# Kernel optimization log

Measured on AMD Instinct MI355X. Metric: run time of the kernel, lower is better.

The kernel has to match this reference:

```python
import jax, jax.numpy as jnp
import numpy as np

B, N, C_IN, D, K = 4, 512, 256, 256, 20


def setup_inputs() -> dict:
    key = jax.random.key(0)
    ks = jax.random.split(key, 6)
    s_in = 1.0 / np.sqrt(C_IN)
    return {
        "x": jax.random.normal(ks[0], (B, N, C_IN), dtype=jnp.float32),
        "edge_index": jnp.zeros((2, 4), dtype=jnp.int64),
        "batch": jnp.zeros((B * N,), dtype=jnp.int64),
        "W_l": jax.random.uniform(ks[1], (D, C_IN), jnp.float32, -s_in, s_in),
        "b_l": jax.random.uniform(ks[2], (D,), jnp.float32, -s_in, s_in),
        "W_r": jax.random.uniform(ks[3], (D, C_IN), jnp.float32, -s_in, s_in),
        "b_r": jax.random.uniform(ks[4], (D,), jnp.float32, -s_in, s_in),
        "att": jax.random.normal(ks[5], (1, D), dtype=jnp.float32) * 0.1,
    }


def reference(x, edge_index, batch, W_l, b_l, W_r, b_r, att):
    b, n, _ = x.shape
    k = K
    # linear projections -> [b, n, d]
    x_l = jnp.einsum("bnc,dc->bnd", x, W_l) + b_l
    x_r = jnp.einsum("bnc,dc->bnd", x, W_r) + b_r
    # pairwise additive attention: [b, n, n, d]
    pair = x_l[:, :, None, :] + x_r[:, None, :, :]
    pair = jnp.where(pair >= 0, pair, 0.2 * pair)  # leaky_relu(0.2)
    alpha = jnp.einsum("bijd,d->bij", pair, att[0])  # [b, n, n]
    alpha = jnp.nan_to_num(alpha, nan=0.0, posinf=0.0, neginf=0.0)
    # knn reduction: topk over last dim
    attention, indices = jax.lax.top_k(alpha, k)  # [b, n, k]
    attention = jax.nn.softmax(attention, axis=-1).reshape(-1)  # [b*n*k]
    # edge index construction with per-batch node offsets
    offset = (jnp.arange(b, dtype=indices.dtype) * n)[:, None]  # [b, 1]
    index_i = jnp.repeat(jnp.arange(n, dtype=indices.dtype), k)[None, :] + offset
    index_j = indices.reshape(b, n * k) + offset
    new_edge_index = jnp.stack([index_i.reshape(-1), index_j.reshape(-1)], axis=0)
    # dropout is identity in eval mode; learn_sys=False -> return directly
    return new_edge_index, attention
```

## Files before the change

kernel.cpp:

```cpp
#include <hip/hip_runtime.h>
#include <math.h>


#define GLD_LDS(gp, lp)                                                        \
    __builtin_amdgcn_global_load_lds(                                          \
        (const __attribute__((address_space(1))) float*)(gp),                  \
        (__attribute__((address_space(3))) float*)(lp), 16, 0, 0)

__global__ __launch_bounds__(256) void k_transpose(const float* __restrict__ x,
        const float* __restrict__ Wl, const float* __restrict__ Wr,
        float* __restrict__ WtL, float* __restrict__ WtR, float* __restrict__ xT) {
    const int g = blockIdx.x, c = threadIdx.x;
    if (g < 256)      WtL[c * 256 + g] = Wl[g * 256 + c];
    else if (g < 512) WtR[c * 256 + (g - 256)] = Wr[(g - 256) * 256 + c];
    else {
        const int r = g - 512;
        xT[(size_t)c * 2048 + r] = x[(size_t)r * 256 + c];
    }
}

__global__ __launch_bounds__(256, 1) void k_proj(const float* __restrict__ xT,
        const float* __restrict__ WtL, const float* __restrict__ WtR,
        const float* __restrict__ bl, const float* __restrict__ br,
        float* __restrict__ XL, float* __restrict__ XRt) {
    __shared__ __align__(16) float xst[256 * 64];
    __shared__ __align__(16) float wst[256 * 64];
    const int tid = threadIdx.x;
    const int lane = tid & 63;
    const int wv = tid >> 6;
    const int g = blockIdx.x;
    const int side = g & 1;
    const int dq = (g >> 1) & 3;
    const int rb = g >> 3;
    const int R = rb * 64;
    const int d0 = dq * 64;
    const int b = R >> 9;
    const float* __restrict__ W = side ? WtR : WtL;

#pragma unroll
    for (int n = 0; n < 16; ++n) {
        const int f4 = (n * 4 + wv) * 64 + lane;
        const int c = f4 >> 4, k4 = f4 & 15;
        GLD_LDS(xT + (size_t)c * 2048 + R + k4 * 4, &xst[(n * 4 + wv) * 256]);
        GLD_LDS(W + (size_t)c * 256 + d0 + k4 * 4, &wst[(n * 4 + wv) * 256]);
    }
    __syncthreads();

    const int rt = tid & 15;
    const int dt = tid >> 4;
    float acc[4][4];
#pragma unroll
    for (int r = 0; r < 4; ++r)
#pragma unroll
        for (int k = 0; k < 4; ++k) acc[r][k] = 0.f;

    const float* xp = &xst[rt * 4];
    const float* wp = &wst[dt * 4];
#pragma unroll 8
    for (int c = 0; c < 256; ++c) {
        const float4 xv = *(const float4*)(xp + c * 64);
        const float4 wq = *(const float4*)(wp + c * 64);
#define PROJ_R(r, XS)                              \
        acc[r][0] = fmaf(XS, wq.x, acc[r][0]);     \
        acc[r][1] = fmaf(XS, wq.y, acc[r][1]);     \
        acc[r][2] = fmaf(XS, wq.z, acc[r][2]);     \
        acc[r][3] = fmaf(XS, wq.w, acc[r][3]);
        PROJ_R(0, xv.x)
        PROJ_R(1, xv.y)
        PROJ_R(2, xv.z)
        PROJ_R(3, xv.w)
#undef PROJ_R
    }

    const float4 bias = *(const float4*)&(side ? br : bl)[d0 + dt * 4];
    if (side == 0) {
#pragma unroll
        for (int r = 0; r < 4; ++r) {
            *(float4*)&XL[(size_t)(R + rt * 4 + r) * 256 + d0 + dt * 4] =
                make_float4(acc[r][0] + bias.x, acc[r][1] + bias.y,
                            acc[r][2] + bias.z, acc[r][3] + bias.w);
        }
    } else {
        const int jr = (R & 511) + rt * 4;
#pragma unroll
        for (int k = 0; k < 4; ++k) {
            const int d = d0 + dt * 4 + k;
            const float bk = k == 0 ? bias.x : k == 1 ? bias.y : k == 2 ? bias.z : bias.w;
            *(float4*)&XRt[((size_t)(b * 256 + d)) * 512 + jr] =
                make_float4(acc[0][k] + bk, acc[1][k] + bk,
                            acc[2][k] + bk, acc[3][k] + bk);
        }
    }
}

__global__ __launch_bounds__(512, 2) void k_pair_topk(const float* __restrict__ XL,
        const float* __restrict__ XRt, const float* __restrict__ att,
        float* __restrict__ out) {
    __shared__ __align__(16) float xls[8 * 256];
    __shared__ __align__(16) float atts[256];
    __shared__ __align__(16) float mrg[3 * 4096];
    __shared__ __align__(16) float mrgb[3 * 512];
    __shared__ float Ais[8];
    const int tid = threadIdx.x;
    const int jc = tid & 127;
    const int h = tid >> 7;
    const int g = blockIdx.x;
    const int R = g * 8, b = R >> 9;

    ((float4*)xls)[tid] = ((const float4*)(XL + (size_t)R * 256))[tid];
    if (tid < 64) ((float4*)atts)[tid] = ((const float4*)att)[tid];
    __syncthreads();

    if (tid < 64) {
        const int ii = tid >> 3, seg = tid & 7;
        const float* xp2 = &xls[ii * 256 + seg * 32];
        const float* ap2 = &atts[seg * 32];
        float p = 0.f;
#pragma unroll
        for (int q = 0; q < 8; ++q) {
            const float4 xv = *(const float4*)(xp2 + q * 4);
            const float4 av = *(const float4*)(ap2 + q * 4);
            p += av.x * xv.x + av.y * xv.y + av.z * xv.z + av.w * xv.w;
        }
        p += __shfl_xor(p, 1); p += __shfl_xor(p, 2); p += __shfl_xor(p, 4);
        if (seg == 0) Ais[ii] = p;
    }

    const int dbase = h * 64;
    const float* __restrict__ xrp = XRt + (size_t)b * 131072 + (size_t)dbase * 512 + jc * 4;

    float acc[8][4];
#pragma unroll
    for (int i = 0; i < 8; ++i)
#pragma unroll
        for (int c = 0; c < 4; ++c) acc[i][c] = 0.f;
    float bacc[4] = {0.f, 0.f, 0.f, 0.f};

    float4 bufA[8], bufB[8];
#pragma unroll
    for (int dd = 0; dd < 8; ++dd) bufA[dd] = *(const float4*)(xrp + (size_t)dd * 512);

#pragma unroll
    for (int ch = 0; ch < 8; ++ch) {
        const float4* cur = (ch & 1) ? bufB : bufA;
        float4* nxt = (ch & 1) ? bufA : bufB;
        if (ch < 7) {
            const float* p = xrp + (size_t)(ch + 1) * 8 * 512;
#pragma unroll
            for (int dd = 0; dd < 8; ++dd) nxt[dd] = *(const float4*)(p + (size_t)dd * 512);
        }
        const int d0 = dbase + ch * 8;
        const float4 at0 = *(const float4*)&atts[d0];
        const float4 at1 = *(const float4*)&atts[d0 + 4];
#define BSTEP(ATC, XR4)                                    \
        bacc[0] = fmaf(ATC, XR4.x, bacc[0]);               \
        bacc[1] = fmaf(ATC, XR4.y, bacc[1]);               \
        bacc[2] = fmaf(ATC, XR4.z, bacc[2]);               \
        bacc[3] = fmaf(ATC, XR4.w, bacc[3]);
        BSTEP(at0.x, cur[0]) BSTEP(at0.y, cur[1]) BSTEP(at0.z, cur[2]) BSTEP(at0.w, cur[3])
        BSTEP(at1.x, cur[4]) BSTEP(at1.y, cur[5]) BSTEP(at1.z, cur[6]) BSTEP(at1.w, cur[7])
#undef BSTEP
#pragma unroll
        for (int i = 0; i < 8; ++i) {
            const float4 xa = *(const float4*)&xls[i * 256 + d0];
            const float4 xb = *(const float4*)&xls[i * 256 + d0 + 4];
#define PSTEP(XLC, ATC, XR4)                                       \
            acc[i][0] = fmaf(ATC, fabsf(XLC + XR4.x), acc[i][0]);   \
            acc[i][1] = fmaf(ATC, fabsf(XLC + XR4.y), acc[i][1]);   \
            acc[i][2] = fmaf(ATC, fabsf(XLC + XR4.z), acc[i][2]);   \
            acc[i][3] = fmaf(ATC, fabsf(XLC + XR4.w), acc[i][3]);
            PSTEP(xa.x, at0.x, cur[0])
            PSTEP(xa.y, at0.y, cur[1])
            PSTEP(xa.z, at0.z, cur[2])
            PSTEP(xa.w, at0.w, cur[3])
            PSTEP(xb.x, at1.x, cur[4])
            PSTEP(xb.y, at1.y, cur[5])
            PSTEP(xb.z, at1.z, cur[6])
            PSTEP(xb.w, at1.w, cur[7])
#undef PSTEP
        }
    }

    if (h) {
        float* m = &mrg[(h - 1) * 4096];
#pragma unroll
        for (int i = 0; i < 8; ++i)
            *(float4*)&m[i * 512 + jc * 4] =
                make_float4(acc[i][0], acc[i][1], acc[i][2], acc[i][3]);
        *(float4*)&mrgb[(h - 1) * 512 + jc * 4] =
            make_float4(bacc[0], bacc[1], bacc[2], bacc[3]);
    }
    __syncthreads();
    if (h == 0) {
        const float4 bm0 = *(const float4*)&mrgb[jc * 4];
        const float4 bm1 = *(const float4*)&mrgb[512 + jc * 4];
        const float4 bm2 = *(const float4*)&mrgb[1024 + jc * 4];
        const float Bf0 = bacc[0] + bm0.x + bm1.x + bm2.x;
        const float Bf1 = bacc[1] + bm0.y + bm1.y + bm2.y;
        const float Bf2 = bacc[2] + bm0.z + bm1.z + bm2.z;
        const float Bf3 = bacc[3] + bm0.w + bm1.w + bm2.w;
#pragma unroll
        for (int i = 0; i < 8; ++i) {
            const float Ai = Ais[i];
            const float4 m0 = *(const float4*)&mrg[i * 512 + jc * 4];
            const float4 m1 = *(const float4*)&mrg[4096 + i * 512 + jc * 4];
            const float4 m2 = *(const float4*)&mrg[8192 + i * 512 + jc * 4];
            float a0 = fmaf(0.4f, acc[i][0] + m0.x + m1.x + m2.x, 0.6f * (Ai + Bf0));
            float a1 = fmaf(0.4f, acc[i][1] + m0.y + m1.y + m2.y, 0.6f * (Ai + Bf1));
            float a2 = fmaf(0.4f, acc[i][2] + m0.z + m1.z + m2.z, 0.6f * (Ai + Bf2));
            float a3 = fmaf(0.4f, acc[i][3] + m0.w + m1.w + m2.w, 0.6f * (Ai + Bf3));
            if (!isfinite(a0)) a0 = 0.f;
            if (!isfinite(a1)) a1 = 0.f;
            if (!isfinite(a2)) a2 = 0.f;
            if (!isfinite(a3)) a3 = 0.f;
            *(float4*)&mrg[i * 512 + jc * 4] = make_float4(a0, a1, a2, a3);
        }
    }
    __syncthreads();

    const int lane = tid & 63;
    const int i = tid >> 6;
    const float* ar = &mrg[i * 512];
    const float4 u0 = *(const float4*)&ar[lane * 8];
    const float4 u1 = *(const float4*)&ar[lane * 8 + 4];
    float v[8] = {u0.x, u0.y, u0.z, u0.w, u1.x, u1.y, u1.z, u1.w};

    float myval = 0.f, mmax = 0.f;
    int myidx = 0;
    for (int sel = 0; sel < 20; ++sel) {
        float bv = v[0]; int bt = 0;
#pragma unroll
        for (int t = 1; t < 8; ++t) { if (v[t] > bv) { bv = v[t]; bt = t; } }
        int bj = lane * 8 + bt;
#pragma unroll
        for (int off = 32; off; off >>= 1) {
            const float ov = __shfl_xor(bv, off);
            const int   oj = __shfl_xor(bj, off);
            if (ov > bv || (ov == bv && oj < bj)) { bv = ov; bj = oj; }
        }
        if (sel == 0) mmax = bv;
        if (lane == sel) { myval = bv; myidx = bj; }
        if ((bj >> 3) == lane) {
            const int bt2 = bj & 7;
#pragma unroll
            for (int t = 0; t < 8; ++t) if (t == bt2) v[t] = -INFINITY;
        }
    }
    const float e = (lane < 20) ? expf(myval - mmax) : 0.f;
    float s = e;
#pragma unroll
    for (int off = 32; off; off >>= 1) s += __shfl_xor(s, off);
    if (lane < 20) {
        const int row = R + i;
        const int base = row * 20 + lane;
        out[base] = (float)row;
        out[40960 + base] = (float)(b * 512 + myidx);
        out[81920 + base] = e / s;
    }
}

extern "C" void kernel_launch(void* const* d_in, const int* in_sizes, int n_in,
                              void* d_out, int out_size, void* d_ws, size_t ws_size,
                              hipStream_t stream) {
    const float* x   = (const float*)d_in[0];
    const float* Wl  = (const float*)d_in[3];
    const float* bl  = (const float*)d_in[4];
    const float* Wr  = (const float*)d_in[5];
    const float* br  = (const float*)d_in[6];
    const float* att = (const float*)d_in[7];

    float* ws  = (float*)d_ws;
    float* WtL = ws;
    float* WtR = ws + 65536;
    float* xT  = ws + 131072;
    float* XL  = ws + 1048576;
    float* XRt = ws + 1572864;
    float* out = (float*)d_out;

    k_transpose<<<dim3(2560), dim3(256), 0, stream>>>(x, Wl, Wr, WtL, WtR, xT);
    k_proj<<<dim3(256), dim3(256), 0, stream>>>(xT, WtL, WtR, bl, br, XL, XRt);
    k_pair_topk<<<dim3(256), dim3(512), 0, stream>>>(XL, XRt, att, out);
}
```

Baseline: 124.1 us.

## Precompute linear attention terms via att-folded weights in transpose kernel

Uses leaky_relu(z) = 0.6z + 0.4|z| to precompute the linear part att·x_l and att·x_r per node. It does this by folding att into the weights (u = W^T att) in a new small kernel and computing the dot products with x in the transpose kernel. This removes the per-block B accumulation (bacc FMAs) and the Ai dot product from the hot pair/top-k kernel, along with their LDS merge. The cost is an extra kernel launch and slightly different float rounding in the linear term.

```diff
diff --git a/kernel.cpp b/kernel.cpp
--- a/kernel.cpp
+++ b/kernel.cpp
@@ -7,16 +7,57 @@
         (const __attribute__((address_space(1))) float*)(gp),                  \
         (__attribute__((address_space(3))) float*)(lp), 16, 0, 0)
 
+__global__ __launch_bounds__(256) void k_uv(const float* __restrict__ Wl,
+        const float* __restrict__ Wr, const float* __restrict__ bl,
+        const float* __restrict__ br, const float* __restrict__ att,
+        float* __restrict__ ul, float* __restrict__ ur, float* __restrict__ cs) {
+    __shared__ float red[4];
+    const int g = blockIdx.x, tid = threadIdx.x;
+    float p;
+    if (g < 512) {
+        const int side = g >> 8, c = g & 255;
+        const float* W = side ? Wr : Wl;
+        p = att[tid] * W[(size_t)tid * 256 + c];
+    } else {
+        const float* bb = (g == 512) ? bl : br;
+        p = att[tid] * bb[tid];
+    }
+#pragma unroll
+    for (int off = 32; off; off >>= 1) p += __shfl_xor(p, off);
+    if ((tid & 63) == 0) red[tid >> 6] = p;
+    __syncthreads();
+    if (tid == 0) {
+        const float s = red[0] + red[1] + red[2] + red[3];
+        if (g < 256) ul[g] = s;
+        else if (g < 512) ur[g - 256] = s;
+        else cs[g - 512] = s;
+    }
+}
+
 __global__ __launch_bounds__(256) void k_transpose(const float* __restrict__ x,
         const float* __restrict__ Wl, const float* __restrict__ Wr,
-        float* __restrict__ WtL, float* __restrict__ WtR, float* __restrict__ xT) {
+        const float* __restrict__ ul, const float* __restrict__ ur,
+        const float* __restrict__ cs,
+        float* __restrict__ WtL, float* __restrict__ WtR, float* __restrict__ xT,
+        float* __restrict__ Av, float* __restrict__ Bv) {
+    __shared__ float red[8];
     const int g = blockIdx.x, c = threadIdx.x;
-    if (g < 256)      WtL[c * 256 + g] = Wl[g * 256 + c];
-    else if (g < 512) WtR[c * 256 + (g - 256)] = Wr[(g - 256) * 256 + c];
-    else {
-        const int r = g - 512;
-        xT[(size_t)c * 2048 + r] = x[(size_t)r * 256 + c];
-    }
+    if (g < 256)      { WtL[c * 256 + g] = Wl[g * 256 + c]; return; }
+    else if (g < 512) { WtR[c * 256 + (g - 256)] = Wr[(g - 256) * 256 + c]; return; }
+    const int r = g - 512;
+    const float xv = x[(size_t)r * 256 + c];
+    xT[(size_t)c * 2048 + r] = xv;
+    float p = xv * ul[c];
+    float q = xv * ur[c];
+#pragma unroll
+    for (int off = 32; off; off >>= 1) {
+        p += __shfl_xor(p, off);
+        q += __shfl_xor(q, off);
+    }
+    if ((c & 63) == 0) { red[c >> 6] = p; red[4 + (c >> 6)] = q; }
+    __syncthreads();
+    if (c == 0) Av[r] = red[0] + red[1] + red[2] + red[3] + cs[0];
+    if (c == 1) Bv[r] = red[4] + red[5] + red[6] + red[7] + cs[1];
 }
 
 __global__ __launch_bounds__(256, 1) void k_proj(const float* __restrict__ xT,
@@ -94,13 +135,13 @@
 }
 
 __global__ __launch_bounds__(512, 2) void k_pair_topk(const float* __restrict__ XL,
-        const float* __restrict__ XRt, const float* __restrict__ att,
+        const float* __restrict__ XRt, const float* __restrict__ Av,
+        const float* __restrict__ Bv, const float* __restrict__ att,
         float* __restrict__ out) {
     __shared__ __align__(16) float xls[8 * 256];
     __shared__ __align__(16) float atts[256];
     __shared__ __align__(16) float mrg[3 * 4096];
-    __shared__ __align__(16) float mrgb[3 * 512];
-    __shared__ float Ais[8];
+    __shared__ __align__(16) float alph[8 * 512];
     const int tid = threadIdx.x;
     const int jc = tid & 127;
     const int h = tid >> 7;
@@ -111,21 +152,6 @@
     if (tid < 64) ((float4*)atts)[tid] = ((const float4*)att)[tid];
     __syncthreads();
 
-    if (tid < 64) {
-        const int ii = tid >> 3, seg = tid & 7;
-        const float* xp2 = &xls[ii * 256 + seg * 32];
-        const float* ap2 = &atts[seg * 32];
-        float p = 0.f;
-#pragma unroll
-        for (int q = 0; q < 8; ++q) {
-            const float4 xv = *(const float4*)(xp2 + q * 4);
-            const float4 av = *(const float4*)(ap2 + q * 4);
-            p += av.x * xv.x + av.y * xv.y + av.z * xv.z + av.w * xv.w;
-        }
-        p += __shfl_xor(p, 1); p += __shfl_xor(p, 2); p += __shfl_xor(p, 4);
-        if (seg == 0) Ais[ii] = p;
-    }
-
     const int dbase = h * 64;
     const float* __restrict__ xrp = XRt + (size_t)b * 131072 + (size_t)dbase * 512 + jc * 4;
 
@@ -134,7 +160,6 @@
     for (int i = 0; i < 8; ++i)
 #pragma unroll
         for (int c = 0; c < 4; ++c) acc[i][c] = 0.f;
-    float bacc[4] = {0.f, 0.f, 0.f, 0.f};
 
     float4 bufA[8], bufB[8];
 #pragma unroll
@@ -152,14 +177,6 @@
         const int d0 = dbase + ch * 8;
         const float4 at0 = *(const float4*)&atts[d0];
         const float4 at1 = *(const float4*)&atts[d0 + 4];
-#define BSTEP(ATC, XR4)                                    \
-        bacc[0] = fmaf(ATC, XR4.x, bacc[0]);               \
-        bacc[1] = fmaf(ATC, XR4.y, bacc[1]);               \
-        bacc[2] = fmaf(ATC, XR4.z, bacc[2]);               \
-        bacc[3] = fmaf(ATC, XR4.w, bacc[3]);
-        BSTEP(at0.x, cur[0]) BSTEP(at0.y, cur[1]) BSTEP(at0.z, cur[2]) BSTEP(at0.w, cur[3])
-        BSTEP(at1.x, cur[4]) BSTEP(at1.y, cur[5]) BSTEP(at1.z, cur[6]) BSTEP(at1.w, cur[7])
-#undef BSTEP
 #pragma unroll
         for (int i = 0; i < 8; ++i) {
             const float4 xa = *(const float4*)&xls[i * 256 + d0];
@@ -187,40 +204,32 @@
         for (int i = 0; i < 8; ++i)
             *(float4*)&m[i * 512 + jc * 4] =
                 make_float4(acc[i][0], acc[i][1], acc[i][2], acc[i][3]);
-        *(float4*)&mrgb[(h - 1) * 512 + jc * 4] =
-            make_float4(bacc[0], bacc[1], bacc[2], bacc[3]);
     }
     __syncthreads();
     if (h == 0) {
-        const float4 bm0 = *(const float4*)&mrgb[jc * 4];
-        const float4 bm1 = *(const float4*)&mrgb[512 + jc * 4];
-        const float4 bm2 = *(const float4*)&mrgb[1024 + jc * 4];
-        const float Bf0 = bacc[0] + bm0.x + bm1.x + bm2.x;
-        const float Bf1 = bacc[1] + bm0.y + bm1.y + bm2.y;
-        const float Bf2 = bacc[2] + bm0.z + bm1.z + bm2.z;
-        const float Bf3 = bacc[3] + bm0.w + bm1.w + bm2.w;
+        const float4 Bj = *(const float4*)&Bv[b * 512 + jc * 4];
 #pragma unroll
         for (int i = 0; i < 8; ++i) {
-            const float Ai = Ais[i];
+            const float Ai = Av[R + i];
             const float4 m0 = *(const float4*)&mrg[i * 512 + jc * 4];
             const float4 m1 = *(const float4*)&mrg[4096 + i * 512 + jc * 4];
             const float4 m2 = *(const float4*)&mrg[8192 + i * 512 + jc * 4];
-            float a0 = fmaf(0.4f, acc[i][0] + m0.x + m1.x + m2.x, 0.6f * (Ai + Bf0));
-            float a1 = fmaf(0.4f, acc[i][1] + m0.y + m1.y + m2.y, 0.6f * (Ai + Bf1));
-            float a2 = fmaf(0.4f, acc[i][2] + m0.z + m1.z + m2.z, 0.6f * (Ai + Bf2));
-            float a3 = fmaf(0.4f, acc[i][3] + m0.w + m1.w + m2.w, 0.6f * (Ai + Bf3));
+            float a0 = fmaf(0.4f, acc[i][0] + m0.x + m1.x + m2.x, 0.6f * (Ai + Bj.x));
+            float a1 = fmaf(0.4f, acc[i][1] + m0.y + m1.y + m2.y, 0.6f * (Ai + Bj.y));
+            float a2 = fmaf(0.4f, acc[i][2] + m0.z + m1.z + m2.z, 0.6f * (Ai + Bj.z));
+            float a3 = fmaf(0.4f, acc[i][3] + m0.w + m1.w + m2.w, 0.6f * (Ai + Bj.w));
             if (!isfinite(a0)) a0 = 0.f;
             if (!isfinite(a1)) a1 = 0.f;
             if (!isfinite(a2)) a2 = 0.f;
             if (!isfinite(a3)) a3 = 0.f;
-            *(float4*)&mrg[i * 512 + jc * 4] = make_float4(a0, a1, a2, a3);
+            *(float4*)&alph[i * 512 + jc * 4] = make_float4(a0, a1, a2, a3);
         }
     }
     __syncthreads();
 
     const int lane = tid & 63;
     const int i = tid >> 6;
-    const float* ar = &mrg[i * 512];
+    const float* ar = &alph[i * 512];
     const float4 u0 = *(const float4*)&ar[lane * 8];
     const float4 u1 = *(const float4*)&ar[lane * 8 + 4];
     float v[8] = {u0.x, u0.y, u0.z, u0.w, u1.x, u1.y, u1.z, u1.w};
@@ -275,9 +284,16 @@
     float* xT  = ws + 131072;
     float* XL  = ws + 1048576;
     float* XRt = ws + 1572864;
+    float* Av  = ws + 2097152;
+    float* Bv  = ws + 2099200;
+    float* ul  = ws + 2101248;
+    float* ur  = ws + 2101504;
+    float* cs  = ws + 2101760;
     float* out = (float*)d_out;
 
-    k_transpose<<<dim3(2560), dim3(256), 0, stream>>>(x, Wl, Wr, WtL, WtR, xT);
+    k_uv<<<dim3(514), dim3(256), 0, stream>>>(Wl, Wr, bl, br, att, ul, ur, cs);
+    k_transpose<<<dim3(2560), dim3(256), 0, stream>>>(x, Wl, Wr, ul, ur, cs,
+                                                      WtL, WtR, xT, Av, Bv);
     k_proj<<<dim3(256), dim3(256), 0, stream>>>(xT, WtL, WtR, bl, br, XL, XRt);
-    k_pair_topk<<<dim3(256), dim3(512), 0, stream>>>(XL, XRt, att, out);
-}
+    k_pair_topk<<<dim3(256), dim3(512), 0, stream>>>(XL, XRt, Av, Bv, att, out);
+}
```

New measurement: 128.5 us. +3.6%, slower.
